# Kernel tuning notes

Measured on AMD Instinct MI355X. Metric: run time of the kernel, lower is better.

Reference implementation:

```python
import jax, jax.numpy as jnp
import numpy as np

HIDDEN = 64
INPUT_DIM = 128
DEMO_DIM = 12
ATT_WIDTH = 1e7  # history_only=True, attention_width=None -> causal


def setup_inputs() -> dict:
    key = jax.random.key(0)
    ks = jax.random.split(key, 8)
    B, T = 4, 512
    inp = {
        "input": jax.random.normal(ks[0], (B, T, INPUT_DIM), dtype=jnp.float32),
        "demo": jax.random.normal(ks[1], (B, DEMO_DIM), dtype=jnp.float32),
        "Wt": jax.random.normal(ks[2], (INPUT_DIM, HIDDEN), dtype=jnp.float32) * 0.08,
        "Wx": jax.random.normal(ks[3], (INPUT_DIM, HIDDEN), dtype=jnp.float32) * 0.08,
        "Wd": jax.random.normal(ks[4], (DEMO_DIM, HIDDEN), dtype=jnp.float32) * 0.25,
        "bh": jnp.zeros((HIDDEN,), dtype=jnp.float32),
        "Wa": jax.random.normal(ks[5], (HIDDEN, 1), dtype=jnp.float32) * 0.12,
        "ba": jnp.zeros((1,), dtype=jnp.float32),
    }
    return inp


def reference(input, demo, Wt, Wx, Wd, bh, Wa, ba):
    B, T, D = input.shape
    # additive attention scores via broadcasted [B,T,T,H] intermediate
    q = (input @ Wt)[:, :, None, :]          # [B,T,1,H]
    k = (input @ Wx)[:, None, :, :]          # [B,1,T,H]
    d = (demo @ Wd)[:, None, None, :]        # [B,1,1,H]
    h = jnp.tanh(q + k + d + bh)             # [B,T,T,H]
    e = (h @ Wa)[..., 0] + ba[0]             # [B,T,T]
    # custom softmax: exp(e - rowmax) BEFORE masking, then mask, then normalize
    e = jnp.exp(e - jnp.max(e, axis=-1, keepdims=True))
    idx = jnp.arange(T, dtype=jnp.float32)
    lower = idx[:, None] - (ATT_WIDTH - 1.0)  # history_only
    upper = lower + ATT_WIDTH
    mask = ((lower <= idx[None, :]) & (idx[None, :] < upper)).astype(e.dtype)
    e = e * mask
    s = jnp.sum(e, axis=-1, keepdims=True)
    e = e / (s + 1e-7)
    v = jnp.einsum('bts,bsd->btd', e, input)  # [B,T,D]
    return (v, e)
```

## Files before the change

### kernel.cpp

```cpp
#include <hip/hip_runtime.h>
#include <math.h>

#define B_ 4
#define T_ 512
#define D_ 128
#define H_ 64
#define DEMO_ 12
#define LOG2E 1.4426950408889634f
#define SC2   (2.0f * LOG2E)

typedef float float4v __attribute__((ext_vector_type(4)));

__global__ __launch_bounds__(256) void prep_kernel(
    const float* __restrict__ input, const float* __restrict__ demo,
    const float* __restrict__ Wt, const float* __restrict__ Wx,
    const float* __restrict__ Wd, const float* __restrict__ bh,
    float* __restrict__ Q, float* __restrict__ K2T)
{
    __shared__ float in_sh[8 * D_];
    int tid  = threadIdx.x;
    int row0 = blockIdx.x * 8;
    int b    = row0 >> 9;

    #pragma unroll
    for (int k = 0; k < 4; ++k)
        in_sh[tid + 256 * k] = input[row0 * D_ + tid + 256 * k];
    __syncthreads();

    int h  = tid & 63;
    int rr = tid >> 6;

    float dB = bh[h];
    #pragma unroll
    for (int kk = 0; kk < DEMO_; ++kk)
        dB = fmaf(demo[b * DEMO_ + kk], Wd[kk * H_ + h], dB);

    float q0 = 0.f, q1 = 0.f, x0 = 0.f, x1 = 0.f;
    #pragma unroll 8
    for (int k = 0; k < D_; ++k) {
        float wt = Wt[k * H_ + h];
        float wx = Wx[k * H_ + h];
        float a0 = in_sh[rr * D_ + k];
        float a1 = in_sh[(rr + 4) * D_ + k];
        q0 = fmaf(a0, wt, q0);
        q1 = fmaf(a1, wt, q1);
        x0 = fmaf(a0, wx, x0);
        x1 = fmaf(a1, wx, x1);
    }

    int ra = row0 + rr, rb = row0 + rr + 4;
    Q[ra * H_ + h] = q0 * SC2;
    Q[rb * H_ + h] = q1 * SC2;
    int ta = ra & (T_ - 1), tb = rb & (T_ - 1);
    K2T[(b * H_ + h) * T_ + ta] = (x0 + dB) * SC2;
    K2T[(b * H_ + h) * T_ + tb] = (x1 + dB) * SC2;
}

__global__ __launch_bounds__(512, 4) void attn_kernel(
    const float* __restrict__ input,
    const float* __restrict__ Qs, const float* __restrict__ K2T,
    const float* __restrict__ Wa, const float* __restrict__ ba,
    float* __restrict__ out_v, float* __restrict__ out_e)
{
    __shared__ float qsh[H_ * 4];
    __shared__ float red_m[8 * 4];
    __shared__ float red_s[8 * 4];
    __shared__ float csh;
    __shared__ float p_sh[T_ * 4];
    __shared__ float partial[4][4 * D_];

    int tid  = threadIdx.x;
    int b    = blockIdx.y;
    int i0   = blockIdx.x * 4;
    int lane = tid & 63, wv = tid >> 6;

    if (tid < 256) {
        int h = tid >> 2, g = tid & 3;
        qsh[tid] = Qs[(size_t)(b * T_ + i0 + g) * H_ + h];
    }
    if (tid < 64) {
        float w = Wa[tid];
        #pragma unroll
        for (int off = 32; off; off >>= 1) w += __shfl_down(w, off, 64);
        if (tid == 0) csh = (ba[0] + w) * LOG2E;
    }
    __syncthreads();

    const int j = tid;
    const float* k2p = K2T + (size_t)b * H_ * T_ + j;

    float acc[4] = {0.f, 0.f, 0.f, 0.f};
    #pragma unroll 2
    for (int h0 = 0; h0 < H_; h0 += 8) {
        float kv[8];
        #pragma unroll
        for (int u = 0; u < 8; ++u)
            kv[u] = k2p[(size_t)(h0 + u) * T_];
        #pragma unroll
        for (int u = 0; u < 8; ++u) {
            int h    = h0 + u;
            float wa = Wa[h];
            float4v q4 = *(const float4v*)&qsh[h * 4];
            #pragma unroll
            for (int g = 0; g < 4; ++g) {
                float ex = __builtin_amdgcn_exp2f(q4[g] + kv[u]);
                float r  = __builtin_amdgcn_rcpf(1.0f + ex);
                acc[g]   = fmaf(wa, r, acc[g]);
            }
        }
    }

    float CL = csh;
    float eg[4], M[4], p[4], S[4];
    #pragma unroll
    for (int g = 0; g < 4; ++g) {
        eg[g] = fmaf(-2.0f * LOG2E, acc[g], CL);
        M[g]  = eg[g];
    }

    #pragma unroll
    for (int off = 32; off; off >>= 1) {
        #pragma unroll
        for (int g = 0; g < 4; ++g) M[g] = fmaxf(M[g], __shfl_down(M[g], off, 64));
    }
    if (lane == 0) ((float4v*)red_m)[wv] = (float4v){M[0], M[1], M[2], M[3]};
    __syncthreads();
    {
        float4v r0 = ((float4v*)red_m)[0];
        #pragma unroll
        for (int w = 1; w < 8; ++w) {
            float4v rw = ((float4v*)red_m)[w];
            #pragma unroll
            for (int g = 0; g < 4; ++g) r0[g] = fmaxf(r0[g], rw[g]);
        }
        #pragma unroll
        for (int g = 0; g < 4; ++g) M[g] = r0[g];
    }

    #pragma unroll
    for (int g = 0; g < 4; ++g) {
        p[g] = __builtin_amdgcn_exp2f(eg[g] - M[g]);
        if (j > i0 + g) p[g] = 0.0f;
        S[g] = p[g];
    }
    *(float4v*)&p_sh[j * 4] = (float4v){p[0], p[1], p[2], p[3]};
    #pragma unroll
    for (int off = 32; off; off >>= 1) {
        #pragma unroll
        for (int g = 0; g < 4; ++g) S[g] += __shfl_down(S[g], off, 64);
    }
    if (lane == 0) ((float4v*)red_s)[wv] = (float4v){S[0], S[1], S[2], S[3]};
    __syncthreads();
    float inv_s[4];
    {
        float4v r0 = ((float4v*)red_s)[0];
        #pragma unroll
        for (int w = 1; w < 8; ++w) {
            float4v rw = ((float4v*)red_s)[w];
            #pragma unroll
            for (int g = 0; g < 4; ++g) r0[g] += rw[g];
        }
        #pragma unroll
        for (int g = 0; g < 4; ++g) inv_s[g] = __builtin_amdgcn_rcpf(r0[g] + 1e-7f);
    }

    #pragma unroll
    for (int g = 0; g < 4; ++g)
        out_e[((size_t)(b * T_ + i0 + g)) * T_ + j] = p[g] * inv_s[g];

    {
        int d  = tid & 127;
        int s4 = tid >> 7;
        const float* inp = input + ((size_t)(b * T_) + s4 * 128) * D_ + d;
        float va[4] = {0.f, 0.f, 0.f, 0.f};
        #pragma unroll 4
        for (int jj = 0; jj < 128; ++jj) {
            float x = inp[(size_t)jj * D_];
            float4v p4 = *(const float4v*)&p_sh[(s4 * 128 + jj) * 4];
            #pragma unroll
            for (int g = 0; g < 4; ++g) va[g] = fmaf(p4[g], x, va[g]);
        }
        #pragma unroll
        for (int g = 0; g < 4; ++g)
            partial[s4][g * D_ + d] = va[g] * inv_s[g];
    }
    __syncthreads();

    {
        int g  = tid >> 7;
        int dd = tid & 127;
        float v = partial[0][g * D_ + dd] + partial[1][g * D_ + dd]
                + partial[2][g * D_ + dd] + partial[3][g * D_ + dd];
        out_v[(size_t)(b * T_ + i0 + g) * D_ + dd] = v;
    }
}

extern "C" void kernel_launch(void* const* d_in, const int* in_sizes, int n_in,
                              void* d_out, int out_size, void* d_ws, size_t ws_size,
                              hipStream_t stream)
{
    const float* input = (const float*)d_in[0];
    const float* demo  = (const float*)d_in[1];
    const float* Wt    = (const float*)d_in[2];
    const float* Wx    = (const float*)d_in[3];
    const float* Wd    = (const float*)d_in[4];
    const float* bh    = (const float*)d_in[5];
    const float* Wa    = (const float*)d_in[6];
    const float* ba    = (const float*)d_in[7];

    float* out_v = (float*)d_out;
    float* out_e = out_v + (size_t)B_ * T_ * D_;

    float* Q   = (float*)d_ws;
    float* K2T = Q + (size_t)B_ * T_ * H_;

    prep_kernel<<<dim3(B_ * T_ / 8), 256, 0, stream>>>(input, demo, Wt, Wx, Wd, bh, Q, K2T);
    attn_kernel<<<dim3(T_ / 4, B_), 512, 0, stream>>>(input, Q, K2T, Wa, ba, out_v, out_e);
}
```

Before: 102.7 us.

## Double attention block threads, splitting query rows across thread halves

The attention kernel now runs 1024 threads per block instead of 512. Each half of the block computes scores for two of the four query rows, so per-thread tanh/exp work halves. The weighted-sum stage splits the key range into 8 chunks of 64 rather than 4 of 128. The aim is more parallelism per block to hide latency in the transcendental-heavy score loop. The cost is duplicated K loads across the two halves, a larger partial buffer, and an 8-way final reduction.

```diff
diff --git a/kernel.cpp b/kernel.cpp
--- a/kernel.cpp
+++ b/kernel.cpp
@@ -10,6 +10,7 @@
 #define SC2   (2.0f * LOG2E)
 
 typedef float float4v __attribute__((ext_vector_type(4)));
+typedef float float2v __attribute__((ext_vector_type(2)));
 
 __global__ __launch_bounds__(256) void prep_kernel(
     const float* __restrict__ input, const float* __restrict__ demo,
@@ -56,23 +57,26 @@
     K2T[(b * H_ + h) * T_ + tb] = (x1 + dB) * SC2;
 }
 
-__global__ __launch_bounds__(512, 4) void attn_kernel(
+__global__ __launch_bounds__(1024, 8) void attn_kernel(
     const float* __restrict__ input,
     const float* __restrict__ Qs, const float* __restrict__ K2T,
     const float* __restrict__ Wa, const float* __restrict__ ba,
     float* __restrict__ out_v, float* __restrict__ out_e)
 {
     __shared__ float qsh[H_ * 4];
-    __shared__ float red_m[8 * 4];
-    __shared__ float red_s[8 * 4];
+    __shared__ float red_m[16 * 2];
+    __shared__ float red_s[16 * 2];
     __shared__ float csh;
     __shared__ float p_sh[T_ * 4];
-    __shared__ float partial[4][4 * D_];
+    __shared__ float partial[8][4 * D_];
 
     int tid  = threadIdx.x;
     int b    = blockIdx.y;
     int i0   = blockIdx.x * 4;
     int lane = tid & 63, wv = tid >> 6;
+    int j    = tid & (T_ - 1);
+    int u    = tid >> 9;
+    int g0   = 2 * u;
 
     if (tid < 256) {
         int h = tid >> 2, g = tid & 3;
@@ -86,111 +90,108 @@
     }
     __syncthreads();
 
-    const int j = tid;
     const float* k2p = K2T + (size_t)b * H_ * T_ + j;
 
-    float acc[4] = {0.f, 0.f, 0.f, 0.f};
+    float acc0 = 0.f, acc1 = 0.f;
     #pragma unroll 2
     for (int h0 = 0; h0 < H_; h0 += 8) {
         float kv[8];
         #pragma unroll
-        for (int u = 0; u < 8; ++u)
-            kv[u] = k2p[(size_t)(h0 + u) * T_];
-        #pragma unroll
-        for (int u = 0; u < 8; ++u) {
-            int h    = h0 + u;
+        for (int uu = 0; uu < 8; ++uu)
+            kv[uu] = k2p[(size_t)(h0 + uu) * T_];
+        #pragma unroll
+        for (int uu = 0; uu < 8; ++uu) {
+            int h    = h0 + uu;
             float wa = Wa[h];
-            float4v q4 = *(const float4v*)&qsh[h * 4];
-            #pragma unroll
-            for (int g = 0; g < 4; ++g) {
-                float ex = __builtin_amdgcn_exp2f(q4[g] + kv[u]);
-                float r  = __builtin_amdgcn_rcpf(1.0f + ex);
-                acc[g]   = fmaf(wa, r, acc[g]);
-            }
-        }
-    }
-
-    float CL = csh;
-    float eg[4], M[4], p[4], S[4];
-    #pragma unroll
-    for (int g = 0; g < 4; ++g) {
-        eg[g] = fmaf(-2.0f * LOG2E, acc[g], CL);
-        M[g]  = eg[g];
-    }
-
+            float2v q2 = *(const float2v*)&qsh[h * 4 + g0];
+            float ex0 = __builtin_amdgcn_exp2f(q2[0] + kv[uu]);
+            float ex1 = __builtin_amdgcn_exp2f(q2[1] + kv[uu]);
+            acc0 = fmaf(wa, __builtin_amdgcn_rcpf(1.0f + ex0), acc0);
+            acc1 = fmaf(wa, __builtin_amdgcn_rcpf(1.0f + ex1), acc1);
+        }
+    }
+
+    float CL  = csh;
+    float eg0 = fmaf(-2.0f * LOG2E, acc0, CL);
+    float eg1 = fmaf(-2.0f * LOG2E, acc1, CL);
+
+    float M0 = eg0, M1 = eg1;
     #pragma unroll
     for (int off = 32; off; off >>= 1) {
-        #pragma unroll
-        for (int g = 0; g < 4; ++g) M[g] = fmaxf(M[g], __shfl_down(M[g], off, 64));
-    }
-    if (lane == 0) ((float4v*)red_m)[wv] = (float4v){M[0], M[1], M[2], M[3]};
+        M0 = fmaxf(M0, __shfl_down(M0, off, 64));
+        M1 = fmaxf(M1, __shfl_down(M1, off, 64));
+    }
+    if (lane == 0) ((float2v*)red_m)[wv] = (float2v){M0, M1};
     __syncthreads();
     {
-        float4v r0 = ((float4v*)red_m)[0];
+        float2v m = ((float2v*)red_m)[u * 8];
         #pragma unroll
         for (int w = 1; w < 8; ++w) {
-            float4v rw = ((float4v*)red_m)[w];
-            #pragma unroll
-            for (int g = 0; g < 4; ++g) r0[g] = fmaxf(r0[g], rw[g]);
-        }
-        #pragma unroll
-        for (int g = 0; g < 4; ++g) M[g] = r0[g];
-    }
-
-    #pragma unroll
-    for (int g = 0; g < 4; ++g) {
-        p[g] = __builtin_amdgcn_exp2f(eg[g] - M[g]);
-        if (j > i0 + g) p[g] = 0.0f;
-        S[g] = p[g];
-    }
-    *(float4v*)&p_sh[j * 4] = (float4v){p[0], p[1], p[2], p[3]};
+            float2v mw = ((float2v*)red_m)[u * 8 + w];
+            m[0] = fmaxf(m[0], mw[0]);
+            m[1] = fmaxf(m[1], mw[1]);
+        }
+        M0 = m[0]; M1 = m[1];
+    }
+
+    float p0 = __builtin_amdgcn_exp2f(eg0 - M0);
+    float p1 = __builtin_amdgcn_exp2f(eg1 - M1);
+    if (j > i0 + g0)     p0 = 0.0f;
+    if (j > i0 + g0 + 1) p1 = 0.0f;
+    *(float2v*)&p_sh[j * 4 + g0] = (float2v){p0, p1};
+    float S0 = p0, S1 = p1;
     #pragma unroll
     for (int off = 32; off; off >>= 1) {
-        #pragma unroll
-        for (int g = 0; g < 4; ++g) S[g] += __shfl_down(S[g], off, 64);
-    }
-    if (lane == 0) ((float4v*)red_s)[wv] = (float4v){S[0], S[1], S[2], S[3]};
-    __syncthreads();
-    float inv_s[4];
+        S0 += __shfl_down(S0, off, 64);
+        S1 += __shfl_down(S1, off, 64);
+    }
+    if (lane == 0) ((float2v*)red_s)[wv] = (float2v){S0, S1};
+    __syncthreads();
+
+    float inv4[4];
     {
-        float4v r0 = ((float4v*)red_s)[0];
+        float2v a = ((float2v*)red_s)[0];
+        float2v c = ((float2v*)red_s)[8];
         #pragma unroll
         for (int w = 1; w < 8; ++w) {
-            float4v rw = ((float4v*)red_s)[w];
-            #pragma unroll
-            for (int g = 0; g < 4; ++g) r0[g] += rw[g];
-        }
-        #pragma unroll
-        for (int g = 0; g < 4; ++g) inv_s[g] = __builtin_amdgcn_rcpf(r0[g] + 1e-7f);
-    }
-
-    #pragma unroll
-    for (int g = 0; g < 4; ++g)
-        out_e[((size_t)(b * T_ + i0 + g)) * T_ + j] = p[g] * inv_s[g];
+            float2v aw = ((float2v*)red_s)[w];
+            float2v cw = ((float2v*)red_s)[8 + w];
+            a[0] += aw[0]; a[1] += aw[1];
+            c[0] += cw[0]; c[1] += cw[1];
+        }
+        inv4[0] = __builtin_amdgcn_rcpf(a[0] + 1e-7f);
+        inv4[1] = __builtin_amdgcn_rcpf(a[1] + 1e-7f);
+        inv4[2] = __builtin_amdgcn_rcpf(c[0] + 1e-7f);
+        inv4[3] = __builtin_amdgcn_rcpf(c[1] + 1e-7f);
+    }
+
+    out_e[((size_t)(b * T_ + i0 + g0))     * T_ + j] = p0 * inv4[g0];
+    out_e[((size_t)(b * T_ + i0 + g0 + 1)) * T_ + j] = p1 * inv4[g0 + 1];
 
     {
         int d  = tid & 127;
-        int s4 = tid >> 7;
-        const float* inp = input + ((size_t)(b * T_) + s4 * 128) * D_ + d;
+        int s8 = tid >> 7;
+        const float* inp = input + ((size_t)(b * T_) + s8 * 64) * D_ + d;
         float va[4] = {0.f, 0.f, 0.f, 0.f};
         #pragma unroll 4
-        for (int jj = 0; jj < 128; ++jj) {
+        for (int jj = 0; jj < 64; ++jj) {
             float x = inp[(size_t)jj * D_];
-            float4v p4 = *(const float4v*)&p_sh[(s4 * 128 + jj) * 4];
+            float4v p4 = *(const float4v*)&p_sh[(s8 * 64 + jj) * 4];
             #pragma unroll
             for (int g = 0; g < 4; ++g) va[g] = fmaf(p4[g], x, va[g]);
         }
         #pragma unroll
         for (int g = 0; g < 4; ++g)
-            partial[s4][g * D_ + d] = va[g] * inv_s[g];
-    }
-    __syncthreads();
-
-    {
+            partial[s8][g * D_ + d] = va[g] * inv4[g];
+    }
+    __syncthreads();
+
+    if (tid < 512) {
         int g  = tid >> 7;
         int dd = tid & 127;
-        float v = partial[0][g * D_ + dd] + partial[1][g * D_ + dd]
-                + partial[2][g * D_ + dd] + partial[3][g * D_ + dd];
+        float v = 0.f;
+        #pragma unroll
+        for (int s = 0; s < 8; ++s) v += partial[s][g * D_ + dd];
         out_v[(size_t)(b * T_ + i0 + g) * D_ + dd] = v;
     }
 }
@@ -215,5 +216,5 @@
     float* K2T = Q + (size_t)B_ * T_ * H_;
 
     prep_kernel<<<dim3(B_ * T_ / 8), 256, 0, stream>>>(input, demo, Wt, Wx, Wd, bh, Q, K2T);
-    attn_kernel<<<dim3(T_ / 4, B_), 512, 0, stream>>>(input, Q, K2T, Wa, ba, out_v, out_e);
+    attn_kernel<<<dim3(T_ / 4, B_), 1024, 0, stream>>>(input, Q, K2T, Wa, ba, out_v, out_e);
 }
```

After: 99.16 us. 1.04x faster.
